# Kernel optimization log

Measured on AMD Instinct MI355X. Metric: run time of the kernel, lower is better.

## Reference

```python
import jax, jax.numpy as jnp
import numpy as np
from math import sqrt

W_SIZE = jnp.array([32, 64, 128, 256, 32, 64, 128, 256], dtype=jnp.int32)  # per-head window

def setup_inputs() -> dict:
    key = jax.random.key(0)
    kq, kk, kv = jax.random.split(key, 3)
    B, L, H, E = 4, 2048, 8, 64
    D = 64
    return {
        "queries": jax.random.normal(kq, (B, L, H, E), dtype=jnp.float32),
        "keys": jax.random.normal(kk, (B, L, H, E), dtype=jnp.float32),
        "values": jax.random.normal(kv, (B, L, H, D), dtype=jnp.float32),
    }

def reference(queries, keys, values):
    B, L, H, E = queries.shape
    scale = 1.0 / sqrt(E)
    # dense scores: [B, H, L, L]
    scores = jnp.einsum('blhe,bshe->bhls', queries, keys)
    # per-head band mask: |i - j| <= w[h]  -> [H, L, L]
    i = jnp.arange(L)
    diff = jnp.abs(i[:, None] - i[None, :])            # [L, L]
    band = diff[None, :, :] <= W_SIZE[:, None, None]   # [H, L, L]
    scores = jnp.where(band[None], scores, -jnp.inf)
    A = jax.nn.softmax(scale * scores, axis=-1)        # dropout p=0 (eval)
    V = jnp.einsum('bhls,bshd->blhd', A, values)
    return V
```

## Files before the change

kernel.cpp:

```cpp
#include <hip/hip_runtime.h>
#include <math.h>


#define LL 2048
#define HH 8
#define EE 64
#define DD 64
#define RS (HH * EE)

typedef __attribute__((ext_vector_type(8))) short short8;
typedef __attribute__((ext_vector_type(4))) float floatx4;
typedef __attribute__((ext_vector_type(4))) _Float16 half4;
typedef __attribute__((ext_vector_type(2))) __fp16 fp16x2;

static __device__ __forceinline__ unsigned f2bf(float f) {
    union { float f; unsigned u; } v; v.f = f;
    return (v.u + 0x7fff + ((v.u >> 16) & 1)) >> 16;
}
static __device__ __forceinline__ unsigned pack2(float a, float b) {
    return f2bf(a) | (f2bf(b) << 16);
}
static __device__ __forceinline__ unsigned packh2(float a, float b) {
    union { fp16x2 h; unsigned u; } v;
    v.h = __builtin_amdgcn_cvt_pkrtz(a, b);
    return v.u;
}

__global__ __launch_bounds__(256, 8) void mwa_prep(
    const float* __restrict__ K, const float* __restrict__ V,
    short* __restrict__ ws)
{
    const int t   = blockIdx.x;
    const int jt  = t & 31;
    const int h   = (t >> 5) & 7;
    const int b   = t >> 8;
    const int j0  = jt << 6;
    const int tid = threadIdx.x;

    const float* Kt = K + ((size_t)(b * LL + j0) * HH + h) * EE;
    const float* Vt = V + ((size_t)(b * LL + j0) * HH + h) * DD;
    short* wsb = ws + (size_t)(b * HH + h) * 262144 + (size_t)jt * 4 * 2048;

    __shared__ float sV[64 * 68];

#pragma unroll
    for (int uu = 0; uu < 2; ++uu) {
        const int u = tid + uu * 256;
        const int row = u >> 3, cg = u & 7;
        const float4* src = (const float4*)(Kt + (size_t)row * RS + cg * 8);
        float4 f0 = src[0], f1 = src[1];
        uint4 o = { pack2(f0.x,f0.y), pack2(f0.z,f0.w),
                    pack2(f1.x,f1.y), pack2(f1.z,f1.w) };
        *(uint4*)&wsb[(row >> 4) * 2048 + (cg >> 2) * 512 + (cg & 3) * 128 + (row & 15) * 8] = o;
    }

    {
        const int row = tid >> 2, dg = (tid & 3) << 4;
        const float4* src = (const float4*)(Vt + (size_t)row * RS + dg);
        float4 f0 = src[0], f1 = src[1], f2 = src[2], f3 = src[3];
        *(float4*)&sV[row * 68 + dg     ] = f0;
        *(float4*)&sV[row * 68 + dg + 4 ] = f1;
        *(float4*)&sV[row * 68 + dg + 8 ] = f2;
        *(float4*)&sV[row * 68 + dg + 12] = f3;
    }
    __syncthreads();
    {
        const int d = tid >> 2, t4 = tid & 3, jp = t4 << 4;
        unsigned o[8];
#pragma unroll
        for (int r = 0; r < 8; ++r)
            o[r] = packh2(sV[(jp + 2 * r) * 68 + d], sV[(jp + 2 * r + 1) * 68 + d]);
        short* dst = &wsb[t4 * 2048 + 1024 + d * 16];
        *(uint4*)(dst    ) = *(uint4*)&o[0];
        *(uint4*)(dst + 8) = *(uint4*)&o[4];
    }
}

__global__ __launch_bounds__(256, 4) void mwa_r14(
    const float* __restrict__ Q,
    const short* __restrict__ ws,
    float* __restrict__ O)
{
    const int tid  = threadIdx.x;
    const int lane = tid & 63;
    const int wv   = tid >> 6;
    const int quad = lane >> 4;
    const int l15  = lane & 15;

    const int gid  = blockIdx.x;
    const int k    = gid >> 8;
    const int c    = gid & 255;
    const int blk5 = c >> 3;
    const int b    = (c >> 1) & 3;
    const int hb   = c & 1;
    const int h    = hb * 4 + k;
    const int w    = 32 << k;
    const int i0w  = blk5 * 64 + wv * 16;

    const float* Qb  = Q + ((size_t)b * LL * HH + h) * EE;
    const short* wsb = ws + (size_t)(b * HH + h) * 262144;
    float*       Ob  = O + ((size_t)b * LL * HH + h) * DD;

    short8 qf0, qf1;
    {
        const float sc = 0.125f;
        const float* qrow = Qb + (size_t)(i0w + l15) * RS + quad * 8;
        float4 a0 = *(const float4*)(qrow);
        float4 a1 = *(const float4*)(qrow + 4);
        float4 b0 = *(const float4*)(qrow + 32);
        float4 b1 = *(const float4*)(qrow + 36);
        union { short8 s; unsigned u[4]; } q0u, q1u;
        q0u.u[0] = pack2(sc*a0.x, sc*a0.y); q0u.u[1] = pack2(sc*a0.z, sc*a0.w);
        q0u.u[2] = pack2(sc*a1.x, sc*a1.y); q0u.u[3] = pack2(sc*a1.z, sc*a1.w);
        q1u.u[0] = pack2(sc*b0.x, sc*b0.y); q1u.u[1] = pack2(sc*b0.z, sc*b0.w);
        q1u.u[2] = pack2(sc*b1.x, sc*b1.y); q1u.u[3] = pack2(sc*b1.z, sc*b1.w);
        qf0 = q0u.s; qf1 = q1u.s;
    }

    const int qb    = i0w;
    const int iq    = i0w + l15;
    const int te_lo = (qb - w) >> 4;
    const int te_hi = (qb + 15 + w) >> 4;
    const int t_lo  = te_lo < 0 ? 0 : te_lo;
    const int t_hi  = te_hi > 127 ? 127 : te_hi;

    const int koff = quad * 128 + l15 * 8;
    const int voff = 1024 + l15 * 16 + quad * 4;

    floatx4 acc[4] = {};
    float lsum = 0.f;

    short8 k0A, k1A, k0B, k1B;
    half4  v0A, v1A, v2A, v3A, v0B, v1B, v2B, v3B;

#define LOADT(S, tt)                                                          \
    {                                                                         \
        const short* base_ = wsb + (size_t)(tt) * 2048;                       \
        k0##S = *(const short8*)(base_ + koff);                               \
        k1##S = *(const short8*)(base_ + koff + 512);                         \
        v0##S = *(const half4*)(base_ + voff);                                \
        v1##S = *(const half4*)(base_ + voff + 256);                          \
        v2##S = *(const half4*)(base_ + voff + 512);                          \
        v3##S = *(const half4*)(base_ + voff + 768);                          \
    }

#define COMPUTET(S, tt)                                                       \
    {                                                                         \
        floatx4 st = {};                                                      \
        st = __builtin_amdgcn_mfma_f32_16x16x32_bf16(k0##S, qf0, st, 0, 0, 0);\
        st = __builtin_amdgcn_mfma_f32_16x16x32_bf16(k1##S, qf1, st, 0, 0, 0);\
        const bool needMask = ((tt) == te_lo) || ((tt) == te_hi);             \
        const int jq = (tt) * 16 + quad * 4;                                  \
        float pr[4];                                                          \
        _Pragma("unroll")                                                     \
        for (int r = 0; r < 4; ++r) {                                         \
            float x = st[r];                                                  \
            if (needMask) {                                                   \
                const int di = iq - (jq + r);                                 \
                x = (di <= w && di >= -w) ? x : -INFINITY;                    \
            }                                                                 \
            pr[r] = __expf(x);                                                \
            lsum += pr[r];                                                    \
        }                                                                     \
        half4 pf;                                                             \
        {                                                                     \
            union { half4 v; unsigned u[2]; } pu;                             \
            pu.u[0] = packh2(pr[0], pr[1]);                                   \
            pu.u[1] = packh2(pr[2], pr[3]);                                   \
            pf = pu.v;                                                        \
        }                                                                     \
        acc[0] = __builtin_amdgcn_mfma_f32_16x16x16f16(pf, v0##S, acc[0], 0, 0, 0); \
        acc[1] = __builtin_amdgcn_mfma_f32_16x16x16f16(pf, v1##S, acc[1], 0, 0, 0); \
        acc[2] = __builtin_amdgcn_mfma_f32_16x16x16f16(pf, v2##S, acc[2], 0, 0, 0); \
        acc[3] = __builtin_amdgcn_mfma_f32_16x16x16f16(pf, v3##S, acc[3], 0, 0, 0); \
    }

    int t = t_lo;
    LOADT(A, t);
    while (t + 1 <= t_hi) {
        LOADT(B, t + 1);
        COMPUTET(A, t);
        if (t + 2 <= t_hi) LOADT(A, t + 2);
        COMPUTET(B, t + 1);
        t += 2;
    }
    if (t <= t_hi) COMPUTET(A, t);

#undef LOADT
#undef COMPUTET

    lsum += __shfl_xor(lsum, 16, 64);
    lsum += __shfl_xor(lsum, 32, 64);
    float rinv[4];
#pragma unroll
    for (int r = 0; r < 4; ++r) {
        const float lr = __shfl(lsum, quad * 4 + r, 64);
        rinv[r] = 1.0f / lr;
    }
#pragma unroll
    for (int nt = 0; nt < 4; ++nt) {
#pragma unroll
        for (int r = 0; r < 4; ++r) {
            Ob[(size_t)(i0w + quad * 4 + r) * RS + nt * 16 + l15]
                = acc[nt][r] * rinv[r];
        }
    }
}

#define K_BUF(cu)  (sAll + (cu) * 4096)
#define V_BUF(cu)  (sAll + 8192 + (cu) * 4608)

static __device__ __forceinline__ void barrier_nodrain() {
    asm volatile("s_waitcnt lgkmcnt(0)" ::: "memory");
    __builtin_amdgcn_s_barrier();
}

static __device__ __forceinline__ void compute_tile72(
    int j0, const short* __restrict__ kbase, const short* __restrict__ vbase,
    int w, int qb, int iq, int quad, int l15,
    short8 qf0, short8 qf1, floatx4* __restrict__ acc, float& lsum)
{
#pragma unroll
    for (int t4 = 0; t4 < 4; ++t4) {
        const int jb = j0 + t4 * 16;
        if (jb > qb + 15 + w || jb + 15 < qb - w) continue;
        const bool needMask = ((jb + 15 - qb) > w) || ((qb + 15 - jb) > w);

        const short* kp = kbase + 1024 * t4 + 128 * quad + 8 * l15;
        short8 k0 = *(const short8*)kp;
        short8 k1 = *(const short8*)(kp + 512);
        floatx4 st = {};
        st = __builtin_amdgcn_mfma_f32_16x16x32_bf16(k0, qf0, st, 0, 0, 0);
        st = __builtin_amdgcn_mfma_f32_16x16x32_bf16(k1, qf1, st, 0, 0, 0);

        float pr[4];
        const int jq = jb + quad * 4;
#pragma unroll
        for (int r = 0; r < 4; ++r) {
            float x = st[r];
            if (needMask) {
                const int di = iq - (jq + r);
                x = (di <= w && di >= -w) ? x : -INFINITY;
            }
            pr[r] = __expf(x);
            lsum += pr[r];
        }
        half4 pf;
        {
            union { half4 v; unsigned u[2]; } pu;
            pu.u[0] = packh2(pr[0], pr[1]);
            pu.u[1] = packh2(pr[2], pr[3]);
            pf = pu.v;
        }
#pragma unroll
        for (int nt = 0; nt < 4; ++nt) {
            half4 vf = *(const half4*)(vbase + (nt * 16 + l15) * 72 + t4 * 16 + quad * 4);
            acc[nt] = __builtin_amdgcn_mfma_f32_16x16x16f16(pf, vf, acc[nt], 0, 0, 0);
        }
    }
}

#define ISSUE_F(jn, kf0_, kf1_, vv_)                                            \
    {                                                                           \
        const float4* src_ = (const float4*)(Kb + (size_t)((jn) + rowp) * RS + cp); \
        kf0_ = src_[0]; kf1_ = src_[1];                                         \
        _Pragma("unroll")                                                       \
        for (int rr_ = 0; rr_ < 8; ++rr_)                                       \
            vv_[rr_] = Vb[(size_t)((jn) + wv * 8 + rr_) * RS + lane];           \
    }
#define STAGE_F(bufIdx, kf0_, kf1_, vv_)                                        \
    {                                                                           \
        uint4 u0_ = { pack2(kf0_.x,kf0_.y), pack2(kf0_.z,kf0_.w),               \
                      pack2(kf1_.x,kf1_.y), pack2(kf1_.z,kf1_.w) };             \
        *(uint4*)&K_BUF(bufIdx)[kWoff] = u0_;                                   \
        uint4 w0_ = { packh2(vv_[0],vv_[1]), packh2(vv_[2],vv_[3]),             \
                      packh2(vv_[4],vv_[5]), packh2(vv_[6],vv_[7]) };           \
        *(uint4*)&V_BUF(bufIdx)[vWoff] = w0_;                                   \
    }

__global__ __launch_bounds__(512, 4) void mwa_r11f(
    const float* __restrict__ Q,
    const float* __restrict__ K,
    const float* __restrict__ V,
    float* __restrict__ O)
{
    const int tid  = threadIdx.x;
    const int lane = tid & 63;
    const int wv   = tid >> 6;
    const int quad = lane >> 4;
    const int l15  = lane & 15;

    const int gid   = blockIdx.x;
    const int heavy = (gid >> 8) == 0;
    const int c     = gid & 255;
    const int it    = c >> 4;
    const int rem   = c & 15;
    const int b     = rem >> 2;
    const int z     = rem & 3;
    const int hb    = z >> 1;
    const int p     = z & 1;
    const int h     = hb * 4 + (heavy ? (3 - p) : p);
    const int i0    = it << 7;
    const int w     = 32 << (h & 3);

    alignas(16) __shared__ short sAll[17408];

    const float* Qb = Q + ((size_t)b * LL * HH + h) * EE;
    const float* Kb = K + ((size_t)b * LL * HH + h) * EE;
    const float* Vb = V + ((size_t)b * LL * HH + h) * DD;
    float*       Ob = O + ((size_t)b * LL * HH + h) * DD;

    {
        const float sc = 0.125f;
        const int row = tid >> 2, cc = (tid & 3) << 4;
        const float4* src = (const float4*)(Qb + (size_t)(i0 + row) * RS + cc);
        float4 f0 = src[0], f1 = src[1], f2 = src[2], f3 = src[3];
        uint4 u0 = { pack2(sc*f0.x,sc*f0.y), pack2(sc*f0.z,sc*f0.w),
                     pack2(sc*f1.x,sc*f1.y), pack2(sc*f1.z,sc*f1.w) };
        uint4 u1 = { pack2(sc*f2.x,sc*f2.y), pack2(sc*f2.z,sc*f2.w),
                     pack2(sc*f3.x,sc*f3.y), pack2(sc*f3.z,sc*f3.w) };
        uint4* dst = (uint4*)&sAll[row * 72 + cc];
        dst[0] = u0; dst[1] = u1;
    }
    __syncthreads();
    short8 qf0, qf1;
    {
        const short* qp = &sAll[(wv * 16 + l15) * 72 + quad * 8];
        qf0 = *(const short8*)qp;
        qf1 = *(const short8*)(qp + 32);
    }
    __syncthreads();

    const int jt_lo = max(0, i0 - w) >> 6;
    const int jt_hi = min(LL - 1, i0 + 127 + w) >> 6;
    const int n     = jt_hi - jt_lo + 1;

    const int rowp  = tid >> 3, cp = (tid & 7) << 3;
    const int jtw   = rowp >> 4, l15w = rowp & 15, ks = cp >> 5, q0w = (cp >> 3) & 3;
    const int kWoff = (((jtw * 2 + ks) * 4 + q0w) * 16 + l15w) * 8;
    const int vWoff = lane * 72 + wv * 8;

    float4 kA0, kA1; float vA[8];
    float4 kB0, kB1; float vB[8];
    ISSUE_F(jt_lo << 6, kA0, kA1, vA);
    STAGE_F(0, kA0, kA1, vA);
    if (n > 1) ISSUE_F((jt_lo + 1) << 6, kA0, kA1, vA);
    __syncthreads();

    floatx4 acc[4] = {};
    float lsum = 0.f;
    const int iq = i0 + wv * 16 + l15;
    const int qb = i0 + wv * 16;

    for (int s = 0; s < n; s += 2) {
        const int jt = jt_lo + s;
        if (s + 2 < n) ISSUE_F((jt + 2) << 6, kB0, kB1, vB);
        if (s + 1 < n) STAGE_F(1, kA0, kA1, vA);
        compute_tile72(jt << 6, K_BUF(0), V_BUF(0), w, qb, iq, quad, l15, qf0, qf1, acc, lsum);
        barrier_nodrain();

        if (s + 1 < n) {
            if (s + 3 < n) ISSUE_F((jt + 3) << 6, kA0, kA1, vA);
            if (s + 2 < n) STAGE_F(0, kB0, kB1, vB);
            compute_tile72((jt + 1) << 6, K_BUF(1), V_BUF(1), w, qb, iq, quad, l15, qf0, qf1, acc, lsum);
            barrier_nodrain();
        }
    }

    lsum += __shfl_xor(lsum, 16, 64);
    lsum += __shfl_xor(lsum, 32, 64);
    float rinv[4];
#pragma unroll
    for (int r = 0; r < 4; ++r) {
        const float lr = __shfl(lsum, quad * 4 + r, 64);
        rinv[r] = 1.0f / lr;
    }
#pragma unroll
    for (int nt = 0; nt < 4; ++nt) {
#pragma unroll
        for (int r = 0; r < 4; ++r) {
            Ob[(size_t)(i0 + wv * 16 + quad * 4 + r) * RS + nt * 16 + l15]
                = acc[nt][r] * rinv[r];
        }
    }
}

extern "C" void kernel_launch(void* const* d_in, const int* in_sizes, int n_in,
                              void* d_out, int out_size, void* d_ws, size_t ws_size,
                              hipStream_t stream)
{
    const float* Q = (const float*)d_in[0];
    const float* K = (const float*)d_in[1];
    const float* V = (const float*)d_in[2];
    float* O = (float*)d_out;

    const size_t wsNeed = (size_t)4 * 8 * 32 * 4 * 2048 * sizeof(short);
    if (ws_size >= wsNeed) {
        short* ws = (short*)d_ws;
        hipLaunchKernelGGL(mwa_prep, dim3(1024), dim3(256), 0, stream, K, V, ws);
        hipLaunchKernelGGL(mwa_r14, dim3(1024), dim3(256), 0, stream, Q, ws, O);
    } else {
        hipLaunchKernelGGL(mwa_r11f, dim3(512), dim3(512), 0, stream, Q, K, V, O);
    }
}
```

Baseline: 110.2 us.

## Use block-uniform tile range with 4-deep register prefetch and per-iteration barrier

```diff
diff --git a/kernel.cpp b/kernel.cpp
--- a/kernel.cpp
+++ b/kernel.cpp
@@ -76,7 +76,7 @@
     }
 }
 
-__global__ __launch_bounds__(256, 4) void mwa_r14(
+__global__ __launch_bounds__(256, 4) void mwa_r15(
     const float* __restrict__ Q,
     const short* __restrict__ ws,
     float* __restrict__ O)
@@ -95,7 +95,8 @@
     const int hb   = c & 1;
     const int h    = hb * 4 + k;
     const int w    = 32 << k;
-    const int i0w  = blk5 * 64 + wv * 16;
+    const int qb0  = blk5 * 64;
+    const int i0w  = qb0 + wv * 16;
 
     const float* Qb  = Q + ((size_t)b * LL * HH + h) * EE;
     const short* wsb = ws + (size_t)(b * HH + h) * 262144;
@@ -117,12 +118,11 @@
         qf0 = q0u.s; qf1 = q1u.s;
     }
 
-    const int qb    = i0w;
-    const int iq    = i0w + l15;
-    const int te_lo = (qb - w) >> 4;
-    const int te_hi = (qb + 15 + w) >> 4;
-    const int t_lo  = te_lo < 0 ? 0 : te_lo;
-    const int t_hi  = te_hi > 127 ? 127 : te_hi;
+    const int t_lo = max(0,  (qb0 - w) >> 4);
+    const int t_hi = min(127, (qb0 + 63 + w) >> 4);
+
+    const int qb = i0w;
+    const int iq = i0w + l15;
 
     const int koff = quad * 128 + l15 * 8;
     const int voff = 1024 + l15 * 16 + quad * 4;
@@ -130,8 +130,9 @@
     floatx4 acc[4] = {};
     float lsum = 0.f;
 
-    short8 k0A, k1A, k0B, k1B;
+    short8 k0A, k1A, k0B, k1B, k0C, k1C, k0D, k1D;
     half4  v0A, v1A, v2A, v3A, v0B, v1B, v2B, v3B;
+    half4  v0C, v1C, v2C, v3C, v0D, v1D, v2D, v3D;
 
 #define LOADT(S, tt)                                                          \
     {                                                                         \
@@ -149,8 +150,9 @@
         floatx4 st = {};                                                      \
         st = __builtin_amdgcn_mfma_f32_16x16x32_bf16(k0##S, qf0, st, 0, 0, 0);\
         st = __builtin_amdgcn_mfma_f32_16x16x32_bf16(k1##S, qf1, st, 0, 0, 0);\
-        const bool needMask = ((tt) == te_lo) || ((tt) == te_hi);             \
-        const int jq = (tt) * 16 + quad * 4;                                  \
+        const int jb = (tt) * 16;                                             \
+        const bool needMask = ((jb + 15 - qb) > w) || ((qb + 15 - jb) > w);   \
+        const int jq = jb + quad * 4;                                         \
         float pr[4];                                                          \
         _Pragma("unroll")                                                     \
         for (int r = 0; r < 4; ++r) {                                         \
@@ -177,14 +179,20 @@
 
     int t = t_lo;
     LOADT(A, t);
-    while (t + 1 <= t_hi) {
-        LOADT(B, t + 1);
+    LOADT(B, t + 1);
+    LOADT(C, t + 2);
+
+    for (; t <= t_hi; t += 4) {
+        __builtin_amdgcn_s_barrier();
+        if (t + 3 <= t_hi) LOADT(D, t + 3);
         COMPUTET(A, t);
-        if (t + 2 <= t_hi) LOADT(A, t + 2);
-        COMPUTET(B, t + 1);
-        t += 2;
-    }
-    if (t <= t_hi) COMPUTET(A, t);
+        if (t + 4 <= t_hi) LOADT(A, t + 4);
+        if (t + 1 <= t_hi) COMPUTET(B, t + 1);
+        if (t + 5 <= t_hi) LOADT(B, t + 5);
+        if (t + 2 <= t_hi) COMPUTET(C, t + 2);
+        if (t + 6 <= t_hi) LOADT(C, t + 6);
+        if (t + 3 <= t_hi) COMPUTET(D, t + 3);
+    }
 
 #undef LOADT
 #undef COMPUTET
@@ -398,7 +406,7 @@
     if (ws_size >= wsNeed) {
         short* ws = (short*)d_ws;
         hipLaunchKernelGGL(mwa_prep, dim3(1024), dim3(256), 0, stream, K, V, ws);
-        hipLaunchKernelGGL(mwa_r14, dim3(1024), dim3(256), 0, stream, Q, ws, O);
+        hipLaunchKernelGGL(mwa_r15, dim3(1024), dim3(256), 0, stream, Q, ws, O);
     } else {
         hipLaunchKernelGGL(mwa_r11f, dim3(512), dim3(512), 0, stream, Q, K, V, O);
     }
```

After: 113.4 us. +2.9%, slower.

## Use atomic-counter persistent scheduling with widest windows first in attention kernel

Applied to the files above, without the earlier changes.

```diff
diff --git a/kernel.cpp b/kernel.cpp
--- a/kernel.cpp
+++ b/kernel.cpp
@@ -76,9 +76,10 @@
     }
 }
 
-__global__ __launch_bounds__(256, 4) void mwa_r14(
+__global__ __launch_bounds__(256, 4) void mwa_r16(
     const float* __restrict__ Q,
     const short* __restrict__ ws,
+    int* __restrict__ ctrs,
     float* __restrict__ O)
 {
     const int tid  = threadIdx.x;
@@ -87,122 +88,133 @@
     const int quad = lane >> 4;
     const int l15  = lane & 15;
 
-    const int gid  = blockIdx.x;
-    const int k    = gid >> 8;
-    const int c    = gid & 255;
-    const int blk5 = c >> 3;
-    const int b    = (c >> 1) & 3;
-    const int hb   = c & 1;
-    const int h    = hb * 4 + k;
-    const int w    = 32 << k;
-    const int i0w  = blk5 * 64 + wv * 16;
-
-    const float* Qb  = Q + ((size_t)b * LL * HH + h) * EE;
-    const short* wsb = ws + (size_t)(b * HH + h) * 262144;
-    float*       Ob  = O + ((size_t)b * LL * HH + h) * DD;
-
-    short8 qf0, qf1;
-    {
-        const float sc = 0.125f;
-        const float* qrow = Qb + (size_t)(i0w + l15) * RS + quad * 8;
-        float4 a0 = *(const float4*)(qrow);
-        float4 a1 = *(const float4*)(qrow + 4);
-        float4 b0 = *(const float4*)(qrow + 32);
-        float4 b1 = *(const float4*)(qrow + 36);
-        union { short8 s; unsigned u[4]; } q0u, q1u;
-        q0u.u[0] = pack2(sc*a0.x, sc*a0.y); q0u.u[1] = pack2(sc*a0.z, sc*a0.w);
-        q0u.u[2] = pack2(sc*a1.x, sc*a1.y); q0u.u[3] = pack2(sc*a1.z, sc*a1.w);
-        q1u.u[0] = pack2(sc*b0.x, sc*b0.y); q1u.u[1] = pack2(sc*b0.z, sc*b0.w);
-        q1u.u[2] = pack2(sc*b1.x, sc*b1.y); q1u.u[3] = pack2(sc*b1.z, sc*b1.w);
-        qf0 = q0u.s; qf1 = q1u.s;
-    }
-
-    const int qb    = i0w;
-    const int iq    = i0w + l15;
-    const int te_lo = (qb - w) >> 4;
-    const int te_hi = (qb + 15 + w) >> 4;
-    const int t_lo  = te_lo < 0 ? 0 : te_lo;
-    const int t_hi  = te_hi > 127 ? 127 : te_hi;
+    const int q  = blockIdx.x & 7;
+    const int b  = q >> 1;
+    const int hb = q & 1;
+    int* ctr = ctrs + q;
+
+    __shared__ int sTask;
 
     const int koff = quad * 128 + l15 * 8;
     const int voff = 1024 + l15 * 16 + quad * 4;
 
-    floatx4 acc[4] = {};
-    float lsum = 0.f;
-
-    short8 k0A, k1A, k0B, k1B;
-    half4  v0A, v1A, v2A, v3A, v0B, v1B, v2B, v3B;
+    for (;;) {
+        __syncthreads();
+        if (tid == 0) sTask = atomicAdd(ctr, 1);
+        __syncthreads();
+        const int tau = sTask;
+        if (tau >= 128) break;
+
+        const int k    = 3 - (tau >> 5);
+        const int band = tau & 31;
+        const int h    = hb * 4 + k;
+        const int w    = 32 << k;
+        const int i0w  = band * 64 + wv * 16;
+
+        const float* Qb  = Q + ((size_t)b * LL * HH + h) * EE;
+        const short* wsb = ws + (size_t)(b * HH + h) * 262144;
+        float*       Ob  = O + ((size_t)b * LL * HH + h) * DD;
+
+        short8 qf0, qf1;
+        {
+            const float sc = 0.125f;
+            const float* qrow = Qb + (size_t)(i0w + l15) * RS + quad * 8;
+            float4 a0 = *(const float4*)(qrow);
+            float4 a1 = *(const float4*)(qrow + 4);
+            float4 b0 = *(const float4*)(qrow + 32);
+            float4 b1 = *(const float4*)(qrow + 36);
+            union { short8 s; unsigned u[4]; } q0u, q1u;
+            q0u.u[0] = pack2(sc*a0.x, sc*a0.y); q0u.u[1] = pack2(sc*a0.z, sc*a0.w);
+            q0u.u[2] = pack2(sc*a1.x, sc*a1.y); q0u.u[3] = pack2(sc*a1.z, sc*a1.w);
+            q1u.u[0] = pack2(sc*b0.x, sc*b0.y); q1u.u[1] = pack2(sc*b0.z, sc*b0.w);
+            q1u.u[2] = pack2(sc*b1.x, sc*b1.y); q1u.u[3] = pack2(sc*b1.z, sc*b1.w);
+            qf0 = q0u.s; qf1 = q1u.s;
+        }
+
+        const int qb    = i0w;
+        const int iq    = i0w + l15;
+        const int te_lo = (qb - w) >> 4;
+        const int te_hi = (qb + 15 + w) >> 4;
+        const int t_lo  = te_lo < 0 ? 0 : te_lo;
+        const int t_hi  = te_hi > 127 ? 127 : te_hi;
+
+        floatx4 acc[4] = {};
+        float lsum = 0.f;
+
+        short8 k0A, k1A, k0B, k1B;
+        half4  v0A, v1A, v2A, v3A, v0B, v1B, v2B, v3B;
 
 #define LOADT(S, tt)                                                          \
-    {                                                                         \
-        const short* base_ = wsb + (size_t)(tt) * 2048;                       \
-        k0##S = *(const short8*)(base_ + koff);                               \
-        k1##S = *(const short8*)(base_ + koff + 512);                         \
-        v0##S = *(const half4*)(base_ + voff);                                \
-        v1##S = *(const half4*)(base_ + voff + 256);                          \
-        v2##S = *(const half4*)(base_ + voff + 512);                          \
-        v3##S = *(const half4*)(base_ + voff + 768);                          \
-    }
+        {                                                                     \
+            const short* base_ = wsb + (size_t)(tt) * 2048;                   \
+            k0##S = *(const short8*)(base_ + koff);                           \
+            k1##S = *(const short8*)(base_ + koff + 512);                     \
+            v0##S = *(const half4*)(base_ + voff);                            \
+            v1##S = *(const half4*)(base_ + voff + 256);                      \
+            v2##S = *(const half4*)(base_ + voff + 512);                      \
+            v3##S = *(const half4*)(base_ + voff + 768);                      \
+        }
 
 #define COMPUTET(S, tt)                                                       \
-    {                                                                         \
-        floatx4 st = {};                                                      \
-        st = __builtin_amdgcn_mfma_f32_16x16x32_bf16(k0##S, qf0, st, 0, 0, 0);\
-        st = __builtin_amdgcn_mfma_f32_16x16x32_bf16(k1##S, qf1, st, 0, 0, 0);\
-        const bool needMask = ((tt) == te_lo) || ((tt) == te_hi);             \
-        const int jq = (tt) * 16 + quad * 4;                                  \
-        float pr[4];                                                          \
-        _Pragma("unroll")                                                     \
-        for (int r = 0; r < 4; ++r) {                                         \
-            float x = st[r];                                                  \
-            if (needMask) {                                                   \
-                const int di = iq - (jq + r);                                 \
-                x = (di <= w && di >= -w) ? x : -INFINITY;                    \
+        {                                                                     \
+            floatx4 st = {};                                                  \
+            st = __builtin_amdgcn_mfma_f32_16x16x32_bf16(k0##S, qf0, st, 0, 0, 0); \
+            st = __builtin_amdgcn_mfma_f32_16x16x32_bf16(k1##S, qf1, st, 0, 0, 0); \
+            const bool needMask = ((tt) == te_lo) || ((tt) == te_hi);         \
+            const int jq = (tt) * 16 + quad * 4;                              \
+            float pr[4];                                                      \
+            _Pragma("unroll")                                                 \
+            for (int r = 0; r < 4; ++r) {                                     \
+                float x = st[r];                                              \
+                if (needMask) {                                               \
+                    const int di = iq - (jq + r);                             \
+                    x = (di <= w && di >= -w) ? x : -INFINITY;                \
+                }                                                             \
+                pr[r] = __expf(x);                                            \
+                lsum += pr[r];                                                \
             }                                                                 \
-            pr[r] = __expf(x);                                                \
-            lsum += pr[r];                                                    \
-        }                                                                     \
-        half4 pf;                                                             \
-        {                                                                     \
-            union { half4 v; unsigned u[2]; } pu;                             \
-            pu.u[0] = packh2(pr[0], pr[1]);                                   \
-            pu.u[1] = packh2(pr[2], pr[3]);                                   \
-            pf = pu.v;                                                        \
-        }                                                                     \
-        acc[0] = __builtin_amdgcn_mfma_f32_16x16x16f16(pf, v0##S, acc[0], 0, 0, 0); \
-        acc[1] = __builtin_amdgcn_mfma_f32_16x16x16f16(pf, v1##S, acc[1], 0, 0, 0); \
-        acc[2] = __builtin_amdgcn_mfma_f32_16x16x16f16(pf, v2##S, acc[2], 0, 0, 0); \
-        acc[3] = __builtin_amdgcn_mfma_f32_16x16x16f16(pf, v3##S, acc[3], 0, 0, 0); \
-    }
-
-    int t = t_lo;
-    LOADT(A, t);
-    while (t + 1 <= t_hi) {
-        LOADT(B, t + 1);
-        COMPUTET(A, t);
-        if (t + 2 <= t_hi) LOADT(A, t + 2);
-        COMPUTET(B, t + 1);
-        t += 2;
-    }
-    if (t <= t_hi) COMPUTET(A, t);
+            half4 pf;                                                         \
+            {                                                                 \
+                union { half4 v; unsigned u[2]; } pu;                         \
+                pu.u[0] = packh2(pr[0], pr[1]);                               \
+                pu.u[1] = packh2(pr[2], pr[3]);                               \
+                pf = pu.v;                                                    \
+            }                                                                 \
+            acc[0] = __builtin_amdgcn_mfma_f32_16x16x16f16(pf, v0##S, acc[0], 0, 0, 0); \
+            acc[1] = __builtin_amdgcn_mfma_f32_16x16x16f16(pf, v1##S, acc[1], 0, 0, 0); \
+            acc[2] = __builtin_amdgcn_mfma_f32_16x16x16f16(pf, v2##S, acc[2], 0, 0, 0); \
+            acc[3] = __builtin_amdgcn_mfma_f32_16x16x16f16(pf, v3##S, acc[3], 0, 0, 0); \
+        }
+
+        int t = t_lo;
+        LOADT(A, t);
+        while (t + 1 <= t_hi) {
+            LOADT(B, t + 1);
+            COMPUTET(A, t);
+            if (t + 2 <= t_hi) LOADT(A, t + 2);
+            COMPUTET(B, t + 1);
+            t += 2;
+        }
+        if (t <= t_hi) COMPUTET(A, t);
 
 #undef LOADT
 #undef COMPUTET
 
-    lsum += __shfl_xor(lsum, 16, 64);
-    lsum += __shfl_xor(lsum, 32, 64);
-    float rinv[4];
-#pragma unroll
-    for (int r = 0; r < 4; ++r) {
-        const float lr = __shfl(lsum, quad * 4 + r, 64);
-        rinv[r] = 1.0f / lr;
-    }
-#pragma unroll
-    for (int nt = 0; nt < 4; ++nt) {
+        lsum += __shfl_xor(lsum, 16, 64);
+        lsum += __shfl_xor(lsum, 32, 64);
+        float rinv[4];
 #pragma unroll
         for (int r = 0; r < 4; ++r) {
-            Ob[(size_t)(i0w + quad * 4 + r) * RS + nt * 16 + l15]
-                = acc[nt][r] * rinv[r];
+            const float lr = __shfl(lsum, quad * 4 + r, 64);
+            rinv[r] = 1.0f / lr;
+        }
+#pragma unroll
+        for (int nt = 0; nt < 4; ++nt) {
+#pragma unroll
+            for (int r = 0; r < 4; ++r) {
+                Ob[(size_t)(i0w + quad * 4 + r) * RS + nt * 16 + l15]
+                    = acc[nt][r] * rinv[r];
+            }
         }
     }
 }
@@ -394,11 +406,14 @@
     const float* V = (const float*)d_in[2];
     float* O = (float*)d_out;
 
-    const size_t wsNeed = (size_t)4 * 8 * 32 * 4 * 2048 * sizeof(short);
+    const size_t imgBytes = (size_t)4 * 8 * 32 * 4 * 2048 * sizeof(short);
+    const size_t wsNeed   = imgBytes + 64;
     if (ws_size >= wsNeed) {
-        short* ws = (short*)d_ws;
+        short* ws  = (short*)d_ws;
+        int*   ctr = (int*)((char*)d_ws + imgBytes);
+        hipMemsetAsync(ctr, 0, 64, stream);
         hipLaunchKernelGGL(mwa_prep, dim3(1024), dim3(256), 0, stream, K, V, ws);
-        hipLaunchKernelGGL(mwa_r14, dim3(1024), dim3(256), 0, stream, Q, ws, O);
+        hipLaunchKernelGGL(mwa_r16, dim3(1024), dim3(256), 0, stream, Q, ws, ctr, O);
     } else {
         hipLaunchKernelGGL(mwa_r11f, dim3(512), dim3(512), 0, stream, Q, K, V, O);
     }
```

After: 127.5 us. 15.7% more time.

## Split key tiles across waves per 16-row query block with LDS reduction

Applied to the files above, without the earlier changes.

```diff
diff --git a/kernel.cpp b/kernel.cpp
--- a/kernel.cpp
+++ b/kernel.cpp
@@ -76,7 +76,7 @@
     }
 }
 
-__global__ __launch_bounds__(256, 4) void mwa_r14(
+__global__ __launch_bounds__(256, 8) void mwa_r17(
     const float* __restrict__ Q,
     const short* __restrict__ ws,
     float* __restrict__ O)
@@ -88,14 +88,18 @@
     const int l15  = lane & 15;
 
     const int gid  = blockIdx.x;
-    const int k    = gid >> 8;
-    const int c    = gid & 255;
-    const int blk5 = c >> 3;
-    const int b    = (c >> 1) & 3;
-    const int hb   = c & 1;
+    const int kk   = gid >> 10;
+    const int k    = 3 - kk;
+    const int x    = gid & 1023;
+    const int q    = x & 7;
+    const int b    = q >> 1;
+    const int hb   = q & 1;
+    const int y    = x >> 3;
+    const int band = y >> 2;
+    const int rg   = y & 3;
     const int h    = hb * 4 + k;
     const int w    = 32 << k;
-    const int i0w  = blk5 * 64 + wv * 16;
+    const int i0b  = band * 64 + rg * 16;
 
     const float* Qb  = Q + ((size_t)b * LL * HH + h) * EE;
     const short* wsb = ws + (size_t)(b * HH + h) * 262144;
@@ -104,7 +108,7 @@
     short8 qf0, qf1;
     {
         const float sc = 0.125f;
-        const float* qrow = Qb + (size_t)(i0w + l15) * RS + quad * 8;
+        const float* qrow = Qb + (size_t)(i0b + l15) * RS + quad * 8;
         float4 a0 = *(const float4*)(qrow);
         float4 a1 = *(const float4*)(qrow + 4);
         float4 b0 = *(const float4*)(qrow + 32);
@@ -117,12 +121,16 @@
         qf0 = q0u.s; qf1 = q1u.s;
     }
 
-    const int qb    = i0w;
-    const int iq    = i0w + l15;
+    const int qb    = i0b;
+    const int iq    = i0b + l15;
     const int te_lo = (qb - w) >> 4;
     const int te_hi = (qb + 15 + w) >> 4;
     const int t_lo  = te_lo < 0 ? 0 : te_lo;
     const int t_hi  = te_hi > 127 ? 127 : te_hi;
+    const int n     = t_hi - t_lo + 1;
+
+    const int tw_lo = t_lo + ((n * wv) >> 2);
+    const int tw_hi = t_lo + ((n * (wv + 1)) >> 2) - 1;
 
     const int koff = quad * 128 + l15 * 8;
     const int voff = 1024 + l15 * 16 + quad * 4;
@@ -154,12 +162,12 @@
         float pr[4];                                                          \
         _Pragma("unroll")                                                     \
         for (int r = 0; r < 4; ++r) {                                         \
-            float x = st[r];                                                  \
+            float xv = st[r];                                                 \
             if (needMask) {                                                   \
                 const int di = iq - (jq + r);                                 \
-                x = (di <= w && di >= -w) ? x : -INFINITY;                    \
+                xv = (di <= w && di >= -w) ? xv : -INFINITY;                  \
             }                                                                 \
-            pr[r] = __expf(x);                                                \
+            pr[r] = __expf(xv);                                               \
             lsum += pr[r];                                                    \
         }                                                                     \
         half4 pf;                                                             \
@@ -175,35 +183,57 @@
         acc[3] = __builtin_amdgcn_mfma_f32_16x16x16f16(pf, v3##S, acc[3], 0, 0, 0); \
     }
 
-    int t = t_lo;
-    LOADT(A, t);
-    while (t + 1 <= t_hi) {
-        LOADT(B, t + 1);
-        COMPUTET(A, t);
-        if (t + 2 <= t_hi) LOADT(A, t + 2);
-        COMPUTET(B, t + 1);
-        t += 2;
-    }
-    if (t <= t_hi) COMPUTET(A, t);
+    if (tw_lo <= tw_hi) {
+        int t = tw_lo;
+        LOADT(A, t);
+        while (t + 1 <= tw_hi) {
+            LOADT(B, t + 1);
+            COMPUTET(A, t);
+            if (t + 2 <= tw_hi) LOADT(A, t + 2);
+            COMPUTET(B, t + 1);
+            t += 2;
+        }
+        if (t <= tw_hi) COMPUTET(A, t);
+    }
 
 #undef LOADT
 #undef COMPUTET
 
-    lsum += __shfl_xor(lsum, 16, 64);
-    lsum += __shfl_xor(lsum, 32, 64);
-    float rinv[4];
-#pragma unroll
-    for (int r = 0; r < 4; ++r) {
-        const float lr = __shfl(lsum, quad * 4 + r, 64);
-        rinv[r] = 1.0f / lr;
-    }
+    __shared__ float accB[4][64][16];
+    __shared__ float lsB[4][64];
 #pragma unroll
     for (int nt = 0; nt < 4; ++nt) {
-#pragma unroll
-        for (int r = 0; r < 4; ++r) {
-            Ob[(size_t)(i0w + quad * 4 + r) * RS + nt * 16 + l15]
-                = acc[nt][r] * rinv[r];
-        }
+        accB[wv][lane][nt * 4 + 0] = acc[nt][0];
+        accB[wv][lane][nt * 4 + 1] = acc[nt][1];
+        accB[wv][lane][nt * 4 + 2] = acc[nt][2];
+        accB[wv][lane][nt * 4 + 3] = acc[nt][3];
+    }
+    lsB[wv][lane] = lsum;
+    __syncthreads();
+
+    {
+        const int row  = tid >> 4;
+        const int colg = tid & 15;
+        float lrow = 0.f;
+#pragma unroll
+        for (int mw = 0; mw < 4; ++mw)
+#pragma unroll
+            for (int qd = 0; qd < 4; ++qd)
+                lrow += lsB[mw][qd * 16 + row];
+        const float rinv = 1.0f / lrow;
+
+        float4 ov;
+        float* ovp = (float*)&ov;
+#pragma unroll
+        for (int c4 = 0; c4 < 4; ++c4) {
+            const int col = colg * 4 + c4;
+            const int sl  = (row >> 2) * 16 + (col & 15);
+            const int si  = (col >> 4) * 4 + (row & 3);
+            float s = accB[0][sl][si] + accB[1][sl][si]
+                    + accB[2][sl][si] + accB[3][sl][si];
+            ovp[c4] = s * rinv;
+        }
+        *(float4*)&Ob[(size_t)(i0b + row) * RS + colg * 4] = ov;
     }
 }
 
@@ -237,12 +267,12 @@
         const int jq = jb + quad * 4;
 #pragma unroll
         for (int r = 0; r < 4; ++r) {
-            float x = st[r];
+            float xv = st[r];
             if (needMask) {
                 const int di = iq - (jq + r);
-                x = (di <= w && di >= -w) ? x : -INFINITY;
+                xv = (di <= w && di >= -w) ? xv : -INFINITY;
             }
-            pr[r] = __expf(x);
+            pr[r] = __expf(xv);
             lsum += pr[r];
         }
         half4 pf;
@@ -394,11 +424,11 @@
     const float* V = (const float*)d_in[2];
     float* O = (float*)d_out;
 
-    const size_t wsNeed = (size_t)4 * 8 * 32 * 4 * 2048 * sizeof(short);
-    if (ws_size >= wsNeed) {
+    const size_t imgBytes = (size_t)4 * 8 * 32 * 4 * 2048 * sizeof(short);
+    if (ws_size >= imgBytes) {
         short* ws = (short*)d_ws;
         hipLaunchKernelGGL(mwa_prep, dim3(1024), dim3(256), 0, stream, K, V, ws);
-        hipLaunchKernelGGL(mwa_r14, dim3(1024), dim3(256), 0, stream, Q, ws, O);
+        hipLaunchKernelGGL(mwa_r17, dim3(4096), dim3(256), 0, stream, Q, ws, O);
     } else {
         hipLaunchKernelGGL(mwa_r11f, dim3(512), dim3(512), 0, stream, Q, K, V, O);
     }
```

New measurement: 155.9 us. +41.5%, slower.
